# Optimization experiments

Measured on AMD Instinct MI355X. Metric: run time of the kernel, lower is better.

The kernel has to match this reference:

```python
import jax, jax.numpy as jnp
import numpy as np

N, T, D = 50000, 16, 4          # nodes, timesteps, input features
E = 800000                      # edges
H, HID = 4, 32                  # GAT heads, hidden dim (concat=False -> mean over heads)
TH, THID = 4, 64                # temporal heads, temporal hidden (= 2*HID)
HD = THID // TH                 # temporal head dim
NEG_SLOPE = 0.2


def setup_inputs() -> dict:
    key = jax.random.key(0)
    ks = iter(jax.random.split(key, 64))
    nrm = lambda shape, s=0.05: jax.random.normal(next(ks), shape, dtype=jnp.float32) * s
    inp = {}
    inp["x"] = jax.random.normal(next(ks), (N, T, D), dtype=jnp.float32)
    inp["edge_index"] = jax.random.randint(next(ks), (2, E), 0, N)
    inp["edge_weight"] = jax.random.uniform(next(ks), (E,), dtype=jnp.float32)
    # input projection
    inp["in_W"], inp["in_b"] = nrm((D, HID)), nrm((HID,))
    # two GATv2 layers (lin_l, lin_r, lin_edge (no bias), att, out bias)
    for i in range(2):
        inp[f"g{i}_Wl"], inp[f"g{i}_bl"] = nrm((HID, H * HID)), nrm((H * HID,))
        inp[f"g{i}_Wr"], inp[f"g{i}_br"] = nrm((HID, H * HID)), nrm((H * HID,))
        inp[f"g{i}_We"] = nrm((1, H * HID))
        inp[f"g{i}_att"] = nrm((H, HID))
        inp[f"g{i}_bias"] = nrm((HID,))
    # temporal attention block
    inp["Wq"], inp["bq"] = nrm((HID, THID)), nrm((THID,))
    inp["Wk"], inp["bk"] = nrm((HID, THID)), nrm((THID,))
    inp["Wv"], inp["bv"] = nrm((HID, THID)), nrm((THID,))
    inp["Wo"], inp["bo"] = nrm((THID, HID)), nrm((HID,))
    # heads
    inp["fW1"], inp["fb1"] = nrm((HID, 32)), nrm((32,))
    inp["fW2"], inp["fb2"] = nrm((32, 1)), nrm((1,))
    inp["rW1"], inp["rb1"] = nrm((HID, 32)), nrm((32,))
    inp["rW2"], inp["rb2"] = nrm((32, 1)), nrm((1,))
    return inp


def _gatv2(xp, edge_index, edge_attr, Wl, bl, Wr, br, We, att, bias):
    """GATv2Conv, heads=H, concat=False (mean), edge_dim=1, no self loops."""
    src, dst = edge_index[0], edge_index[1]          # message src -> dst
    xl = (xp @ Wl + bl).reshape(N, H, HID)
    xr = (xp @ Wr + br).reshape(N, H, HID)
    ee = (edge_attr @ We).reshape(E, H, HID)
    m = xl[src] + xr[dst] + ee                       # (E,H,C)
    m = jnp.where(m > 0, m, NEG_SLOPE * m)           # leaky_relu
    logits = jnp.einsum('ehc,hc->eh', m, att)        # (E,H)
    mx = jax.ops.segment_max(logits, dst, num_segments=N)
    mx = jnp.where(jnp.isfinite(mx), mx, 0.0)
    a = jnp.exp(logits - mx[dst])
    denom = jax.ops.segment_sum(a, dst, num_segments=N)
    alpha = a / (denom[dst] + 1e-16)                 # segment softmax over dst
    out = jax.ops.segment_sum(alpha[:, :, None] * xl[src], dst, num_segments=N)
    return out.mean(axis=1) + bias                   # (N,HID)


def reference(x, edge_index, edge_weight,
              in_W, in_b,
              g0_Wl, g0_bl, g0_Wr, g0_br, g0_We, g0_att, g0_bias,
              g1_Wl, g1_bl, g1_Wr, g1_br, g1_We, g1_att, g1_bias,
              Wq, bq, Wk, bk, Wv, bv, Wo, bo,
              fW1, fb1, fW2, fb2, rW1, rb1, rW2, rb2):
    edge_attr = edge_weight[:, None]                 # (E,1)
    x_seq = x @ in_W + in_b                          # (N,T,HID)
    x_pool = x_seq.mean(axis=1)                      # (N,HID)
    x_pool = jax.nn.relu(_gatv2(x_pool, edge_index, edge_attr,
                                g0_Wl, g0_bl, g0_Wr, g0_br, g0_We, g0_att, g0_bias))
    x_pool = jax.nn.relu(_gatv2(x_pool, edge_index, edge_attr,
                                g1_Wl, g1_bl, g1_Wr, g1_br, g1_We, g1_att, g1_bias))
    x_seq = x_seq + x_pool[:, None, :]
    node_reps = jnp.transpose(x_seq, (1, 0, 2))      # (T,N,HID)

    def heads(z):                                    # (T,N,THID) -> (N,TH,T,HD)
        return jnp.transpose(z.reshape(T, N, TH, HD), (1, 2, 0, 3))
    Qh = heads(node_reps @ Wq + bq)
    Kh = heads(node_reps @ Wk + bk)
    Vh = heads(node_reps @ Wv + bv)
    scale = HD ** -0.5
    scores = jnp.einsum('bhtd,bhsd->bhts', Qh, Kh) * scale
    w = jax.nn.softmax(scores, axis=-1)
    ctx = jnp.einsum('bhts,bhsd->bhtd', w, Vh)       # (N,TH,T,HD)
    ctx = jnp.transpose(ctx, (2, 0, 1, 3)).reshape(T, N, THID)
    temporal_out = ctx @ Wo + bo                     # (T,N,HID)

    last = temporal_out[-1]                          # (N,HID)
    forecast = jax.nn.relu(jax.nn.relu(last @ fW1 + fb1) @ fW2 + fb2)   # (N,1)
    risk = jax.nn.sigmoid(jax.nn.relu(last @ rW1 + rb1) @ rW2 + rb2)    # (N,1)
    return forecast, risk, temporal_out
```

## Files before the change

kernel.cpp:

```cpp
#include <hip/hip_runtime.h>
#include <hip/hip_bf16.h>

#define NN 50000
#define TT 16
#define DD 4
#define EE 800000
#define HH 4
#define HID 32
#define THID 64
#define HD 16

typedef __attribute__((ext_vector_type(8))) short bf16x8;
typedef __attribute__((ext_vector_type(4))) float f32x4;
typedef __attribute__((ext_vector_type(4))) unsigned u32x4;

__device__ __forceinline__ unsigned short f2bf(float f){
    unsigned u = __float_as_uint(f);
    u = u + 0x7fffu + ((u >> 16) & 1u);
    return (unsigned short)(u >> 16);
}
__device__ __forceinline__ unsigned pk2(float a, float b){
    return (unsigned)f2bf(a) | ((unsigned)f2bf(b) << 16);
}
__device__ __forceinline__ bf16x8 mk8(unsigned a0, unsigned a1, unsigned a2, unsigned a3){
    u32x4 u = {a0, a1, a2, a3};
    return __builtin_bit_cast(bf16x8, u);
}
__device__ __forceinline__ bf16x8 gather8(int d0, int d1, int s0, int s1, bool zero){
    int a0 = __shfl(d0, s0, 64);
    int a1 = __shfl(d1, s0, 64);
    int a2 = __shfl(d0, s1, 64);
    int a3 = __shfl(d1, s1, 64);
    if (zero){ a0 = 0; a1 = 0; a2 = 0; a3 = 0; }
    return mk8((unsigned)a0, (unsigned)a1, (unsigned)a2, (unsigned)a3);
}

__global__ __launch_bounds__(256) void pool_kernel(const float* __restrict__ x,
        const float* __restrict__ in_W, const float* __restrict__ in_b,
        float* __restrict__ xp){
    __shared__ float xs[512];
    __shared__ float xb[8][4];
    int tid = threadIdx.x;
    size_t base = (size_t)blockIdx.x * 512;
    xs[tid]       = x[base + tid];
    xs[tid + 256] = x[base + tid + 256];
    __syncthreads();
    if (tid < 32){
        int nl = tid >> 2, d = tid & 3;
        float s = 0.f;
        #pragma unroll
        for (int t = 0; t < 16; t++) s += xs[nl*64 + t*4 + d];
        xb[nl][d] = s * (1.f/16.f);
    }
    __syncthreads();
    int nl = tid >> 5, c = tid & 31;
    float v = in_b[c];
    #pragma unroll
    for (int d = 0; d < 4; d++) v += xb[nl][d] * in_W[d*32 + c];
    xp[(size_t)(blockIdx.x*8 + nl)*32 + c] = v;
}

__global__ void wfrag_kernel(const float* __restrict__ Wq, const float* __restrict__ Wk,
                             const float* __restrict__ Wv, const float* __restrict__ Wo,
                             unsigned short* __restrict__ frag){
    int fid = blockIdx.x, lane = threadIdx.x;
    const float* W; int b, k0, ncol;
    if (fid < 4)      { W = Wq; b = fid;      k0 = 0;  ncol = 64; }
    else if (fid < 8) { W = Wk; b = fid - 4;  k0 = 0;  ncol = 64; }
    else if (fid < 12){ W = Wv; b = fid - 8;  k0 = 0;  ncol = 64; }
    else { W = Wo; int rb = (fid-12) >> 1, ks = (fid-12) & 1; b = rb; k0 = ks*32; ncol = 32; }
    int col = 16*b + (lane & 15);
    int kk  = k0 + (lane >> 4)*8;
    unsigned short* out = frag + ((size_t)fid*64 + lane)*8;
    #pragma unroll
    for (int j = 0; j < 8; j++) out[j] = f2bf(W[(size_t)(kk + j)*ncol + col]);
}

__global__ void count_kernel(const int* __restrict__ ei, int* __restrict__ counts){
    int e = blockIdx.x*256 + threadIdx.x;
    if (e >= EE) return;
    atomicAdd(&counts[ei[EE + e]], 1);
}

#define SBLK 49

__global__ __launch_bounds__(256) void bsum_kernel(const int* __restrict__ counts,
                                                   int* __restrict__ bsum){
    int b = blockIdx.x, tid = threadIdx.x;
    int base = b*1024 + tid*4;
    int s = 0;
    if (base + 3 < NN){ int4 v = *(const int4*)(counts + base); s = v.x+v.y+v.z+v.w; }
    else { for (int i = 0; i < 4; i++) if (base+i < NN) s += counts[base+i]; }
    #pragma unroll
    for (int off = 1; off < 64; off <<= 1) s += __shfl_xor(s, off, 64);
    __shared__ int wsum[4];
    if ((tid & 63) == 0) wsum[tid >> 6] = s;
    __syncthreads();
    if (tid == 0) bsum[b] = wsum[0] + wsum[1] + wsum[2] + wsum[3];
}

__global__ __launch_bounds__(256) void scan2_kernel(const int* __restrict__ counts,
                                                    const int* __restrict__ bsum,
                                                    int* __restrict__ offs,
                                                    int* __restrict__ nxt){
    int b = blockIdx.x, tid = threadIdx.x;
    __shared__ int lds[256];
    __shared__ int bofs_s;
    if (tid < 64){
        int v = (tid < b) ? bsum[tid] : 0;
        #pragma unroll
        for (int off = 1; off < 64; off <<= 1) v += __shfl_xor(v, off, 64);
        if (tid == 0) bofs_s = v;
    }
    int base = b*1024 + tid*4;
    int c0=0, c1=0, c2=0, c3=0;
    if (base + 3 < NN){ int4 v = *(const int4*)(counts + base); c0=v.x; c1=v.y; c2=v.z; c3=v.w; }
    else {
        if (base   < NN) c0 = counts[base];
        if (base+1 < NN) c1 = counts[base+1];
        if (base+2 < NN) c2 = counts[base+2];
        if (base+3 < NN) c3 = counts[base+3];
    }
    lds[tid] = c0 + c1 + c2 + c3;
    __syncthreads();
    for (int off = 1; off < 256; off <<= 1){
        int v = (tid >= off) ? lds[tid - off] : 0;
        __syncthreads();
        lds[tid] += v;
        __syncthreads();
    }
    int run = bofs_s + ((tid == 0) ? 0 : lds[tid - 1]);
    if (base   < NN){ offs[base]   = run; nxt[base]   = run; } run += c0;
    if (base+1 < NN){ offs[base+1] = run; nxt[base+1] = run; } run += c1;
    if (base+2 < NN){ offs[base+2] = run; nxt[base+2] = run; } run += c2;
    if (base+3 < NN){ offs[base+3] = run; nxt[base+3] = run; }
    if (b == 0 && tid == 0) offs[NN] = EE;
}

__global__ void fill_kernel(const int* __restrict__ ei, const float* __restrict__ ew,
                            int* __restrict__ nxt, int2* __restrict__ esrc){
    int e = blockIdx.x*256 + threadIdx.x;
    if (e >= EE) return;
    int dst = ei[EE + e];
    int pos = atomicAdd(&nxt[dst], 1);
    esrc[pos] = make_int2(ei[e], __float_as_int(ew[e]));
}

#define LNODES 8
__global__ __launch_bounds__(128) void linlr_kernel(const float* __restrict__ xp,
        const float* __restrict__ Wl, const float* __restrict__ bl,
        const float* __restrict__ Wr, const float* __restrict__ br,
        unsigned short* __restrict__ xlb, float* __restrict__ xr){
    int j = threadIdx.x;
    int n0 = blockIdx.x * LNODES;
    float wl[32], wrr[32];
    #pragma unroll
    for (int k = 0; k < 32; k++){ wl[k] = Wl[k*128 + j]; wrr[k] = Wr[k*128 + j]; }
    float blv = bl[j], brv = br[j];
    __shared__ float xs[LNODES][32];
    int r = j >> 5, c = j & 31;
    #pragma unroll
    for (int q = 0; q < LNODES/4; q++)
        xs[q*4 + r][c] = xp[(size_t)(n0 + q*4 + r)*32 + c];
    __syncthreads();
    #pragma unroll
    for (int m = 0; m < LNODES; m++){
        float al = blv, ar = brv;
        #pragma unroll
        for (int k = 0; k < 32; k++){ float v = xs[m][k]; al += v*wl[k]; ar += v*wrr[k]; }
        xlb[(size_t)(n0+m)*128 + j] = f2bf(al);
        xr[(size_t)(n0+m)*128 + j] = ar;
    }
}

__global__ __launch_bounds__(256) void gat_fused_kernel(
        const int* __restrict__ offs, const int2* __restrict__ esrc,
        const unsigned short* __restrict__ xlb, const float* __restrict__ xr,
        const float* __restrict__ We, const float* __restrict__ att,
        const float* __restrict__ bias, float* __restrict__ xq){
    int n = blockIdx.x;
    int tid = threadIdx.x;
    int w = tid >> 6, lane = tid & 63;
    int c2 = lane << 1;
    float2 xrv  = *(const float2*)(xr + (size_t)n*128 + c2);
    float2 Wev  = *(const float2*)(We + c2);
    float2 attv = *(const float2*)(att + c2);
    int beg = offs[n], end = offs[n+1];
    float acc0 = 0.f, acc1 = 0.f, den = 0.f;
    for (int i = beg + w; i < end; i += 4){
        int2 r = esrc[i];
        int src  = r.x;
        float wt = __int_as_float(r.y);
        unsigned u = *(const unsigned*)(xlb + (size_t)src*128 + c2);
        float xl0 = __uint_as_float(u << 16);
        float xl1 = __uint_as_float(u & 0xffff0000u);
        float m0 = xl0 + xrv.x + wt*Wev.x; m0 = m0 > 0.f ? m0 : 0.2f*m0;
        float m1 = xl1 + xrv.y + wt*Wev.y; m1 = m1 > 0.f ? m1 : 0.2f*m1;
        float z = m0*attv.x + m1*attv.y;
        z += __shfl_xor(z, 1);
        z += __shfl_xor(z, 2);
        z += __shfl_xor(z, 4);
        z += __shfl_xor(z, 8);
        float a = __expf(z);
        den += a; acc0 += a*xl0; acc1 += a*xl1;
    }
    __shared__ float lacc[4][64][2];
    __shared__ float lden[4][64];
    lacc[w][lane][0] = acc0;
    lacc[w][lane][1] = acc1;
    lden[w][lane] = den;
    __syncthreads();
    if (tid < 32){
        float s = 0.f;
        #pragma unroll
        for (int h = 0; h < 4; h++){
            int l = 16*h + (tid >> 1), sl = tid & 1;
            float a = lacc[0][l][sl] + lacc[1][l][sl] + lacc[2][l][sl] + lacc[3][l][sl];
            float d = lden[0][l] + lden[1][l] + lden[2][l] + lden[3][l];
            s += a / (d + 1e-16f);
        }
        s = s*0.25f + bias[tid];
        xq[(size_t)n*32 + tid] = fmaxf(s, 0.f);
    }
}

__global__ __launch_bounds__(256) void temporal_kernel(const float* __restrict__ x,
        const float* __restrict__ xpool,
        const float* __restrict__ in_W, const float* __restrict__ in_b,
        const float* __restrict__ bq, const float* __restrict__ bk,
        const float* __restrict__ bv, const float* __restrict__ bo,
        const unsigned short* __restrict__ wfrag,
        float* __restrict__ out2){
    __shared__ float ctxL[4][64][18];
    int tid = threadIdx.x, w = tid >> 6, lane = tid & 63;
    int n = blockIdx.x*4 + w;
    int t = lane & 15, g = lane >> 4;
    int k0 = g * 8;

    f32x4 xv  = *(const f32x4*)(x + (size_t)n*64 + t*4);
    f32x4 ib0 = *(const f32x4*)(in_b + k0);
    f32x4 ib1 = *(const f32x4*)(in_b + k0 + 4);
    f32x4 xp0 = *(const f32x4*)(xpool + (size_t)n*32 + k0);
    f32x4 xp1 = *(const f32x4*)(xpool + (size_t)n*32 + k0 + 4);
    f32x4 iw0a = *(const f32x4*)(in_W + k0),      iw0b = *(const f32x4*)(in_W + k0 + 4);
    f32x4 iw1a = *(const f32x4*)(in_W + 32 + k0), iw1b = *(const f32x4*)(in_W + 32 + k0 + 4);
    f32x4 iw2a = *(const f32x4*)(in_W + 64 + k0), iw2b = *(const f32x4*)(in_W + 64 + k0 + 4);
    f32x4 iw3a = *(const f32x4*)(in_W + 96 + k0), iw3b = *(const f32x4*)(in_W + 96 + k0 + 4);
    f32x4 sA = ib0 + xp0 + xv[0]*iw0a + xv[1]*iw1a + xv[2]*iw2a + xv[3]*iw3a;
    f32x4 sB = ib1 + xp1 + xv[0]*iw0b + xv[1]*iw1b + xv[2]*iw2b + xv[3]*iw3b;
    bf16x8 sfrag = mk8(pk2(sA[0],sA[1]), pk2(sA[2],sA[3]), pk2(sB[0],sB[1]), pk2(sB[2],sB[3]));

    const bf16x8* WF = (const bf16x8*)wfrag;
    f32x4 zero = {0.f, 0.f, 0.f, 0.f};

    int qd0[4], qd1[4], kd0[4], kd1[4], vd0[4], vd1[4];
    #pragma unroll
    for (int b = 0; b < 4; b++){
        bf16x8 wq = WF[(0*4 + b)*64 + lane];
        bf16x8 wk = WF[(1*4 + b)*64 + lane];
        bf16x8 wv = WF[(2*4 + b)*64 + lane];
        f32x4 qc = __builtin_amdgcn_mfma_f32_16x16x32_bf16(wq, sfrag, zero, 0, 0, 0);
        f32x4 kc = __builtin_amdgcn_mfma_f32_16x16x32_bf16(wk, sfrag, zero, 0, 0, 0);
        f32x4 vc = __builtin_amdgcn_mfma_f32_16x16x32_bf16(sfrag, wv, zero, 0, 0, 0);
        f32x4 bq4 = *(const f32x4*)(bq + 16*b + 4*g);
        f32x4 bk4 = *(const f32x4*)(bk + 16*b + 4*g);
        float bvv = bv[16*b + t];
        qc += bq4; kc += bk4;
        vc[0] += bvv; vc[1] += bvv; vc[2] += bvv; vc[3] += bvv;
        qd0[b] = (int)pk2(qc[0], qc[1]); qd1[b] = (int)pk2(qc[2], qc[3]);
        kd0[b] = (int)pk2(kc[0], kc[1]); kd1[b] = (int)pk2(kc[2], kc[3]);
        vd0[b] = (int)pk2(vc[0], vc[1]); vd1[b] = (int)pk2(vc[2], vc[3]);
    }

    int s0l = t + 32*(g & 1);
    int s1l = s0l + 16;
    bool hiz = (g >= 2);
    #pragma unroll
    for (int h = 0; h < 4; h++){
        bf16x8 ka = gather8(kd0[h], kd1[h], s0l, s1l, hiz);
        bf16x8 qb = gather8(qd0[h], qd1[h], s0l, s1l, hiz);
        f32x4 sc = __builtin_amdgcn_mfma_f32_16x16x32_bf16(ka, qb, zero, 0, 0, 0);
        sc *= 0.25f;
        float m = fmaxf(fmaxf(sc[0], sc[1]), fmaxf(sc[2], sc[3]));
        m = fmaxf(m, __shfl_xor(m, 16, 64));
        m = fmaxf(m, __shfl_xor(m, 32, 64));
        float p0 = __expf(sc[0] - m), p1 = __expf(sc[1] - m);
        float p2 = __expf(sc[2] - m), p3 = __expf(sc[3] - m);
        float sum = p0 + p1 + p2 + p3;
        sum += __shfl_xor(sum, 16, 64);
        sum += __shfl_xor(sum, 32, 64);
        float inv = 1.f / sum;
        int pd0 = (int)pk2(p0, p1), pd1 = (int)pk2(p2, p3);
        bf16x8 va = gather8(vd0[h], vd1[h], s0l, s1l, hiz);
        bf16x8 pb = gather8(pd0, pd1, s0l, s1l, hiz);
        f32x4 cx = __builtin_amdgcn_mfma_f32_16x16x32_bf16(va, pb, zero, 0, 0, 0);
        cx *= inv;
        #pragma unroll
        for (int r = 0; r < 4; r++) ctxL[w][h*16 + 4*g + r][t] = cx[r];
    }

    bf16x8 cb[2];
    #pragma unroll
    for (int ks = 0; ks < 2; ks++){
        float c0 = ctxL[w][ks*32 + k0 + 0][t], c1 = ctxL[w][ks*32 + k0 + 1][t];
        float c2 = ctxL[w][ks*32 + k0 + 2][t], c3 = ctxL[w][ks*32 + k0 + 3][t];
        float c4 = ctxL[w][ks*32 + k0 + 4][t], c5 = ctxL[w][ks*32 + k0 + 5][t];
        float c6 = ctxL[w][ks*32 + k0 + 6][t], c7 = ctxL[w][ks*32 + k0 + 7][t];
        cb[ks] = mk8(pk2(c0,c1), pk2(c2,c3), pk2(c4,c5), pk2(c6,c7));
    }
    #pragma unroll
    for (int rb = 0; rb < 2; rb++){
        bf16x8 wo0 = WF[(12 + rb*2 + 0)*64 + lane];
        bf16x8 wo1 = WF[(12 + rb*2 + 1)*64 + lane];
        f32x4 oc = __builtin_amdgcn_mfma_f32_16x16x32_bf16(wo0, cb[0], zero, 0, 0, 0);
        oc = __builtin_amdgcn_mfma_f32_16x16x32_bf16(wo1, cb[1], oc, 0, 0, 0);
        f32x4 bo4 = *(const f32x4*)(bo + 16*rb + 4*g);
        oc += bo4;
        #pragma unroll
        for (int r = 0; r < 4; r++) ctxL[w][16*rb + 4*g + r][t] = oc[r];
    }
    float o[8];
    #pragma unroll
    for (int j = 0; j < 8; j++) o[j] = ctxL[w][g*8 + j][t];
    float* outp = out2 + ((size_t)t*NN + n)*32 + g*8;
    *(f32x4*)outp       = (f32x4){o[0], o[1], o[2], o[3]};
    *((f32x4*)outp + 1) = (f32x4){o[4], o[5], o[6], o[7]};
}

__global__ __launch_bounds__(256) void head_kernel(const float* __restrict__ out2,
        const float* __restrict__ fW1, const float* __restrict__ fb1,
        const float* __restrict__ fW2, const float* __restrict__ fb2,
        const float* __restrict__ rW1, const float* __restrict__ rb1,
        const float* __restrict__ rW2, const float* __restrict__ rb2,
        float* __restrict__ out0, float* __restrict__ out1){
    int tid = threadIdx.x;
    int wv = tid >> 6, lane = tid & 63;
    int n = blockIdx.x*4 + wv;
    int c = lane & 31, path = lane >> 5;
    const float* W1 = path ? rW1 : fW1;
    const float* b1 = path ? rb1 : fb1;
    const float* W2 = path ? rW2 : fW2;
    const float* b2 = path ? rb2 : fb2;
    const float* last = out2 + ((size_t)15*NN + n)*32;
    float h1 = b1[c];
    #pragma unroll
    for (int k = 0; k < 32; k++) h1 += last[k] * W1[k*32 + c];
    h1 = fmaxf(h1, 0.f);
    float z = h1 * W2[c];
    #pragma unroll
    for (int off = 16; off >= 1; off >>= 1) z += __shfl_xor(z, off, 64);
    if (lane == 0)  out0[n] = fmaxf(z + b2[0], 0.f);
    if (lane == 32) out1[n] = 1.f / (1.f + __expf(-(z + b2[0])));
}

extern "C" void kernel_launch(void* const* d_in, const int* in_sizes, int n_in,
                              void* d_out, int out_size, void* d_ws, size_t ws_size,
                              hipStream_t stream){
    const float* x    = (const float*)d_in[0];
    const int*   ei   = (const int*)  d_in[1];
    const float* ew   = (const float*)d_in[2];
    const float* in_W = (const float*)d_in[3];
    const float* in_b = (const float*)d_in[4];
    const float* Wq = (const float*)d_in[19];
    const float* bq = (const float*)d_in[20];
    const float* Wk = (const float*)d_in[21];
    const float* bk = (const float*)d_in[22];
    const float* Wv = (const float*)d_in[23];
    const float* bv = (const float*)d_in[24];
    const float* Wo = (const float*)d_in[25];
    const float* bo = (const float*)d_in[26];
    const float* fW1 = (const float*)d_in[27];
    const float* fb1 = (const float*)d_in[28];
    const float* fW2 = (const float*)d_in[29];
    const float* fb2 = (const float*)d_in[30];
    const float* rW1 = (const float*)d_in[31];
    const float* rb1 = (const float*)d_in[32];
    const float* rW2 = (const float*)d_in[33];
    const float* rb2 = (const float*)d_in[34];

    float* out0 = (float*)d_out;
    float* out1 = out0 + NN;
    float* out2 = out0 + 2*NN;

    float* ws = (float*)d_ws;
    size_t off = 0;
    unsigned short* xlb = (unsigned short*)(ws + off); off += (size_t)NN*64;
    float* xr     = ws + off; off += (size_t)NN*128;
    float* xpA    = ws + off; off += (size_t)NN*32;
    float* xpB    = ws + off; off += (size_t)NN*32;
    int* counts   = (int*)(ws + off); off += NN;
    int* offs     = (int*)(ws + off); off += NN + 1;
    int* nxt      = (int*)(ws + off); off += NN + 1;
    int* bsum     = (int*)(ws + off); off += SBLK;
    off = (off + 1) & ~(size_t)1;
    int2* esrc    = (int2*)(ws + off); off += (size_t)EE*2;
    off = (off + 3) & ~(size_t)3;
    unsigned short* wfrag = (unsigned short*)(ws + off); off += 16*64*8/2;

    hipMemsetAsync(counts, 0, NN*sizeof(int), stream);
    pool_kernel<<<NN/8, 256, 0, stream>>>(x, in_W, in_b, xpA);
    wfrag_kernel<<<16, 64, 0, stream>>>(Wq, Wk, Wv, Wo, wfrag);
    count_kernel<<<(EE+255)/256, 256, 0, stream>>>(ei, counts);
    bsum_kernel<<<SBLK, 256, 0, stream>>>(counts, bsum);
    scan2_kernel<<<SBLK, 256, 0, stream>>>(counts, bsum, offs, nxt);
    fill_kernel<<<(EE+255)/256, 256, 0, stream>>>(ei, ew, nxt, esrc);

    for (int layer = 0; layer < 2; layer++){
        const float* Wl   = (const float*)d_in[5 + 7*layer];
        const float* bl   = (const float*)d_in[6 + 7*layer];
        const float* Wr   = (const float*)d_in[7 + 7*layer];
        const float* br   = (const float*)d_in[8 + 7*layer];
        const float* We   = (const float*)d_in[9 + 7*layer];
        const float* att  = (const float*)d_in[10 + 7*layer];
        const float* bias = (const float*)d_in[11 + 7*layer];
        const float* xin  = layer ? xpB : xpA;
        float*       xout = layer ? xpA : xpB;
        linlr_kernel<<<NN/LNODES, 128, 0, stream>>>(xin, Wl, bl, Wr, br, xlb, xr);
        gat_fused_kernel<<<NN, 256, 0, stream>>>(offs, esrc, xlb, xr, We, att, bias, xout);
    }

    temporal_kernel<<<NN/4, 256, 0, stream>>>(x, xpA, in_W, in_b,
                                              bq, bk, bv, bo, wfrag, out2);
    head_kernel<<<NN/4, 256, 0, stream>>>(out2, fW1, fb1, fW2, fb2,
                                          rW1, rb1, rW2, rb2, out0, out1);
}
```

Before: 460.9 us.

## Use fp16 for GAT features and process two edges per wavefront

Stores the xl and xr projections as fp16 instead of bf16/fp32 and computes the GATv2 message, leaky-relu and attention dot product with packed half-precision vector math. Each wavefront now handles two edges at once, with 32 lanes per edge and 4 channels per lane, which halves loop trips and cuts the shuffle reduction by one step. The aim is less gather bandwidth and ALU work per edge. The cost is reduced precision in the logits (fp16 range and rounding) and a predicated tail for odd edge counts.

```diff
diff --git a/kernel.cpp b/kernel.cpp
--- a/kernel.cpp
+++ b/kernel.cpp
@@ -12,7 +12,9 @@
 
 typedef __attribute__((ext_vector_type(8))) short bf16x8;
 typedef __attribute__((ext_vector_type(4))) float f32x4;
+typedef __attribute__((ext_vector_type(2))) float f32x2;
 typedef __attribute__((ext_vector_type(4))) unsigned u32x4;
+typedef __attribute__((ext_vector_type(4))) _Float16 h4;
 
 __device__ __forceinline__ unsigned short f2bf(float f){
     unsigned u = __float_as_uint(f);
@@ -150,7 +152,7 @@
 __global__ __launch_bounds__(128) void linlr_kernel(const float* __restrict__ xp,
         const float* __restrict__ Wl, const float* __restrict__ bl,
         const float* __restrict__ Wr, const float* __restrict__ br,
-        unsigned short* __restrict__ xlb, float* __restrict__ xr){
+        _Float16* __restrict__ xlh, _Float16* __restrict__ xrh){
     int j = threadIdx.x;
     int n0 = blockIdx.x * LNODES;
     float wl[32], wrr[32];
@@ -168,59 +170,77 @@
         float al = blv, ar = brv;
         #pragma unroll
         for (int k = 0; k < 32; k++){ float v = xs[m][k]; al += v*wl[k]; ar += v*wrr[k]; }
-        xlb[(size_t)(n0+m)*128 + j] = f2bf(al);
-        xr[(size_t)(n0+m)*128 + j] = ar;
+        xlh[(size_t)(n0+m)*128 + j] = (_Float16)al;
+        xrh[(size_t)(n0+m)*128 + j] = (_Float16)ar;
     }
 }
 
 __global__ __launch_bounds__(256) void gat_fused_kernel(
         const int* __restrict__ offs, const int2* __restrict__ esrc,
-        const unsigned short* __restrict__ xlb, const float* __restrict__ xr,
+        const _Float16* __restrict__ xlh, const _Float16* __restrict__ xrh,
         const float* __restrict__ We, const float* __restrict__ att,
         const float* __restrict__ bias, float* __restrict__ xq){
     int n = blockIdx.x;
     int tid = threadIdx.x;
     int w = tid >> 6, lane = tid & 63;
-    int c2 = lane << 1;
-    float2 xrv  = *(const float2*)(xr + (size_t)n*128 + c2);
-    float2 Wev  = *(const float2*)(We + c2);
-    float2 attv = *(const float2*)(att + c2);
+    int half = lane >> 5, l2 = lane & 31;
+    int cb = (l2 >> 3)*32 + (l2 & 7)*4;
+
+    h4 xr4 = __builtin_bit_cast(h4, *(const f32x2*)(xrh + (size_t)n*128 + cb));
+    f32x4 wef = {We[cb], We[cb+1], We[cb+2], We[cb+3]};
+    h4 We4 = {(_Float16)wef[0], (_Float16)wef[1], (_Float16)wef[2], (_Float16)wef[3]};
+    f32x4 atf = {att[cb], att[cb+1], att[cb+2], att[cb+3]};
+    h4 at4 = {(_Float16)atf[0], (_Float16)atf[1], (_Float16)atf[2], (_Float16)atf[3]};
+
     int beg = offs[n], end = offs[n+1];
-    float acc0 = 0.f, acc1 = 0.f, den = 0.f;
-    for (int i = beg + w; i < end; i += 4){
-        int2 r = esrc[i];
+    float acc0 = 0.f, acc1 = 0.f, acc2 = 0.f, acc3 = 0.f, den = 0.f;
+    for (int i = beg + 2*w; i < end; i += 8){
+        int e = i + half;
+        bool valid = e < end;
+        int ec = valid ? e : end - 1;
+        int2 r = esrc[ec];
         int src  = r.x;
         float wt = __int_as_float(r.y);
-        unsigned u = *(const unsigned*)(xlb + (size_t)src*128 + c2);
-        float xl0 = __uint_as_float(u << 16);
-        float xl1 = __uint_as_float(u & 0xffff0000u);
-        float m0 = xl0 + xrv.x + wt*Wev.x; m0 = m0 > 0.f ? m0 : 0.2f*m0;
-        float m1 = xl1 + xrv.y + wt*Wev.y; m1 = m1 > 0.f ? m1 : 0.2f*m1;
-        float z = m0*attv.x + m1*attv.y;
+        h4 xl4 = __builtin_bit_cast(h4, *(const f32x2*)(xlh + (size_t)src*128 + cb));
+        h4 m = xl4 + xr4 + We4 * (_Float16)wt;
+        h4 rr = __builtin_elementwise_max(m, m * (_Float16)0.2f);
+        h4 zp = at4 * rr;
+        float z = (float)zp[0] + (float)zp[1] + (float)zp[2] + (float)zp[3];
         z += __shfl_xor(z, 1);
         z += __shfl_xor(z, 2);
         z += __shfl_xor(z, 4);
-        z += __shfl_xor(z, 8);
-        float a = __expf(z);
-        den += a; acc0 += a*xl0; acc1 += a*xl1;
-    }
-    __shared__ float lacc[4][64][2];
+        float a = valid ? __expf(z) : 0.f;
+        den  += a;
+        acc0 += a * (float)xl4[0];
+        acc1 += a * (float)xl4[1];
+        acc2 += a * (float)xl4[2];
+        acc3 += a * (float)xl4[3];
+    }
+    __shared__ float lacc[4][64][4];
     __shared__ float lden[4][64];
     lacc[w][lane][0] = acc0;
     lacc[w][lane][1] = acc1;
+    lacc[w][lane][2] = acc2;
+    lacc[w][lane][3] = acc3;
     lden[w][lane] = den;
     __syncthreads();
     if (tid < 32){
+        int j = tid;
         float s = 0.f;
         #pragma unroll
         for (int h = 0; h < 4; h++){
-            int l = 16*h + (tid >> 1), sl = tid & 1;
-            float a = lacc[0][l][sl] + lacc[1][l][sl] + lacc[2][l][sl] + lacc[3][l][sl];
-            float d = lden[0][l] + lden[1][l] + lden[2][l] + lden[3][l];
-            s += a / (d + 1e-16f);
+            int lb = h*8 + (j >> 2);
+            int sub = j & 3;
+            float av = 0.f, dv = 0.f;
+            #pragma unroll
+            for (int ww = 0; ww < 4; ww++){
+                av += lacc[ww][lb][sub] + lacc[ww][lb + 32][sub];
+                dv += lden[ww][lb] + lden[ww][lb + 32];
+            }
+            s += av / (dv + 1e-16f);
         }
-        s = s*0.25f + bias[tid];
-        xq[(size_t)n*32 + tid] = fmaxf(s, 0.f);
+        s = s*0.25f + bias[j];
+        xq[(size_t)n*32 + j] = fmaxf(s, 0.f);
     }
 }
 
@@ -384,8 +404,8 @@
 
     float* ws = (float*)d_ws;
     size_t off = 0;
-    unsigned short* xlb = (unsigned short*)(ws + off); off += (size_t)NN*64;
-    float* xr     = ws + off; off += (size_t)NN*128;
+    _Float16* xlh = (_Float16*)(ws + off); off += (size_t)NN*64;
+    _Float16* xrh = (_Float16*)(ws + off); off += (size_t)NN*64;
     float* xpA    = ws + off; off += (size_t)NN*32;
     float* xpB    = ws + off; off += (size_t)NN*32;
     int* counts   = (int*)(ws + off); off += NN;
@@ -415,8 +435,8 @@
         const float* bias = (const float*)d_in[11 + 7*layer];
         const float* xin  = layer ? xpB : xpA;
         float*       xout = layer ? xpA : xpB;
-        linlr_kernel<<<NN/LNODES, 128, 0, stream>>>(xin, Wl, bl, Wr, br, xlb, xr);
-        gat_fused_kernel<<<NN, 256, 0, stream>>>(offs, esrc, xlb, xr, We, att, bias, xout);
+        linlr_kernel<<<NN/LNODES, 128, 0, stream>>>(xin, Wl, bl, Wr, br, xlh, xrh);
+        gat_fused_kernel<<<NN, 256, 0, stream>>>(offs, esrc, xlh, xrh, We, att, bias, xout);
     }
 
     temporal_kernel<<<NN/4, 256, 0, stream>>>(x, xpA, in_W, in_b,
```

Result: faster. 404.4 us (-12.3%).
